# Optimization experiments

Hardware: AMD Instinct MI355X
Metric: run time of the kernel (lower is better)

The kernel has to match this reference:

```python
import jax, jax.numpy as jnp
import numpy as np

L, H, D, V, T, B = 12, 12, 768, 50257, 1024, 2
HD = D // H


def _ln(x, w, b):
    m = jnp.mean(x, axis=-1, keepdims=True)
    v = jnp.var(x, axis=-1, keepdims=True)
    return (x - m) * jax.lax.rsqrt(v + 1e-5) * w + b


def setup_inputs() -> dict:
    key = jax.random.key(0)
    ks = jax.random.split(key, 8)
    def n(k, shape, std=0.02):
        return jax.random.normal(k, shape, jnp.float32) * std
    return dict(
        x=jax.random.randint(ks[0], (B, T), 0, V),
        wte=n(ks[1], (V, D), 0.01),
        wpe=n(ks[2], (T, D), 0.01),
        ln1_w=jnp.ones((L, D), jnp.float32), ln1_b=jnp.zeros((L, D), jnp.float32),
        qkv_w=n(ks[3], (L, D, 3 * D)), qkv_b=jnp.zeros((L, 3 * D), jnp.float32),
        proj_w=n(ks[4], (L, D, D)), proj_b=jnp.zeros((L, D), jnp.float32),
        ln2_w=jnp.ones((L, D), jnp.float32), ln2_b=jnp.zeros((L, D), jnp.float32),
        fc_w=n(ks[5], (L, D, 4 * D)), fc_b=jnp.zeros((L, 4 * D), jnp.float32),
        fcp_w=n(ks[6], (L, 4 * D, D)), fcp_b=jnp.zeros((L, D), jnp.float32),
        lnf_w=jnp.ones((D,), jnp.float32), lnf_b=jnp.zeros((D,), jnp.float32),
    )


def reference(x, wte, wpe, ln1_w, ln1_b, qkv_w, qkv_b, proj_w, proj_b,
              ln2_w, ln2_b, fc_w, fc_b, fcp_w, fcp_b, lnf_w, lnf_b):
    Bn, Tn = x.shape
    h = wte[x] + wpe[:Tn]                                   # [B,T,D]
    mask = jnp.tril(jnp.ones((Tn, Tn), bool))               # causal mask
    scale = 1.0 / np.sqrt(HD).astype(np.float32)

    def block(h, p):
        l1w, l1b, qw, qb, pw, pb, l2w, l2b, fw, fb, p2w, p2b = p
        a = _ln(h, l1w, l1b)
        qkv = a @ qw + qb                                    # [B,T,3D]
        q, k, v = jnp.split(qkv, 3, axis=-1)
        q = q.reshape(Bn, Tn, H, HD)
        k = k.reshape(Bn, Tn, H, HD)
        v = v.reshape(Bn, Tn, H, HD)
        att = jnp.einsum('bqhd,bkhd->bhqk', q, k) * scale    # [B,H,T,T]
        att = jnp.where(mask, att, -jnp.inf)
        att = jax.nn.softmax(att, axis=-1)
        y = jnp.einsum('bhqk,bkhd->bqhd', att, v).reshape(Bn, Tn, D)
        h = h + y @ pw + pb
        m = _ln(h, l2w, l2b)
        m = jax.nn.gelu(m @ fw + fb, approximate=True)       # tanh GELU
        h = h + m @ p2w + p2b
        return h, None

    h, _ = jax.lax.scan(block, h, (ln1_w, ln1_b, qkv_w, qkv_b, proj_w, proj_b,
                                   ln2_w, ln2_b, fc_w, fc_b, fcp_w, fcp_b))
    logits = _ln(h, lnf_w, lnf_b) @ wte.T                    # tied lm_head
    return logits
```

## Files before the change

kernel.cpp:

```cpp
#include <hip/hip_runtime.h>
#include <hip/hip_bf16.h>

typedef __hip_bfloat16 hbf16;
using bf16x8 = __attribute__((ext_vector_type(8))) __bf16;
using f32x4 = __attribute__((ext_vector_type(4))) float;

constexpr int Lc = 12, Hc = 12, Dc = 768, Vc = 50257, Tc = 1024, Bc = 2, HDc = 64;
constexpr int Mc = Bc * Tc;
constexpr int Vpad = 50304;

constexpr size_t SZ_Q = (size_t)3 * Dc * Dc;
constexpr size_t SZ_P = (size_t)Dc * Dc;
constexpr size_t SZ_F = (size_t)4 * Dc * Dc;
constexpr size_t SZ_FP = (size_t)4 * Dc * Dc;
constexpr size_t SZL = SZ_Q + SZ_P + SZ_F + SZ_FP;
constexpr int NPART = Bc * Hc * 8 * 2;

#define GLD16(gp, lp)                                               \
    __builtin_amdgcn_global_load_lds(                               \
        (__attribute__((address_space(1))) void*)(void*)(gp),       \
        (__attribute__((address_space(3))) void*)(void*)(lp), 16, 0, 0)

__global__ void embed_kernel(const int* __restrict__ x, const float* __restrict__ wte,
                             const float* __restrict__ wpe, float* __restrict__ h) {
    int i = blockIdx.x * blockDim.x + threadIdx.x;
    if (i >= Mc * Dc) return;
    int m = i / Dc, d = i - m * Dc;
    int t = m % Tc;
    int tok = x[m];
    h[i] = wte[(size_t)tok * Dc + d] + wpe[(size_t)t * Dc + d];
}

__global__ __launch_bounds__(256) void ln_kernel(const float* __restrict__ x,
                                                 const float* __restrict__ w,
                                                 const float* __restrict__ b,
                                                 hbf16* __restrict__ out) {
    int wv = threadIdx.x >> 6, lane = threadIdx.x & 63;
    int row = blockIdx.x * 4 + wv;
    const float4* xr = (const float4*)(x + (size_t)row * Dc);
    float4 v[3];
    float s = 0.f, sq = 0.f;
#pragma unroll
    for (int i = 0; i < 3; i++) {
        v[i] = xr[i * 64 + lane];
        s += v[i].x + v[i].y + v[i].z + v[i].w;
        sq += v[i].x * v[i].x + v[i].y * v[i].y + v[i].z * v[i].z + v[i].w * v[i].w;
    }
#pragma unroll
    for (int o = 32; o > 0; o >>= 1) {
        s += __shfl_xor(s, o, 64);
        sq += __shfl_xor(sq, o, 64);
    }
    float mean = s * (1.f / Dc);
    float var = sq * (1.f / Dc) - mean * mean;
    float rstd = rsqrtf(var + 1e-5f);
#pragma unroll
    for (int i = 0; i < 3; i++) {
        int c = (i * 64 + lane) * 4;
        float4 wv4 = *(const float4*)(w + c);
        float4 bv4 = *(const float4*)(b + c);
        float r0 = (v[i].x - mean) * rstd * wv4.x + bv4.x;
        float r1 = (v[i].y - mean) * rstd * wv4.y + bv4.y;
        float r2 = (v[i].z - mean) * rstd * wv4.z + bv4.z;
        float r3 = (v[i].w - mean) * rstd * wv4.w + bv4.w;
        __bf16 q0 = (__bf16)r0, q1 = (__bf16)r1, q2 = (__bf16)r2, q3 = (__bf16)r3;
        ushort4 u;
        u.x = *(unsigned short*)&q0; u.y = *(unsigned short*)&q1;
        u.z = *(unsigned short*)&q2; u.w = *(unsigned short*)&q3;
        *(ushort4*)(out + (size_t)row * Dc + c) = u;
    }
}

__global__ __launch_bounds__(256) void transpose4_kernel(
    const float* __restrict__ s0, const float* __restrict__ s1,
    const float* __restrict__ s2, const float* __restrict__ s3,
    hbf16* __restrict__ d0, hbf16* __restrict__ d1,
    hbf16* __restrict__ d2, hbf16* __restrict__ d3) {
    int id = blockIdx.x;
    size_t lz = blockIdx.y;
    int bx, by, K, N;
    const float* W;
    hbf16* Wt;
    if (id < 1728)      { int t = id;        bx = t % 72; by = t / 72; K = 768;  N = 2304; W = s0 + lz * SZ_Q;  Wt = d0 + lz * SZL; }
    else if (id < 2304) { int t = id - 1728; bx = t % 24; by = t / 24; K = 768;  N = 768;  W = s1 + lz * SZ_P;  Wt = d1 + lz * SZL; }
    else if (id < 4608) { int t = id - 2304; bx = t % 96; by = t / 96; K = 768;  N = 3072; W = s2 + lz * SZ_F;  Wt = d2 + lz * SZL; }
    else                { int t = id - 4608; bx = t % 24; by = t / 24; K = 3072; N = 768;  W = s3 + lz * SZ_FP; Wt = d3 + lz * SZL; }

    __shared__ float tile[32][33];
    int n0 = bx * 32, k0 = by * 32;
    int tx = threadIdx.x & 31, ty = threadIdx.x >> 5;
#pragma unroll
    for (int i = 0; i < 4; i++) {
        int r = ty + i * 8;
        tile[r][tx] = W[(size_t)(k0 + r) * N + n0 + tx];
    }
    __syncthreads();
#pragma unroll
    for (int i = 0; i < 4; i++) {
        int r = ty + i * 8;
        Wt[(size_t)(n0 + r) * K + k0 + tx] = __float2bfloat16(tile[tx][r]);
    }
}

__global__ void convert_wte(const float* __restrict__ wte, hbf16* __restrict__ out) {
    size_t i4 = ((size_t)blockIdx.x * 256 + threadIdx.x) * 4;
    if (i4 >= (size_t)Vpad * Dc) return;
    if (i4 < (size_t)Vc * Dc) {
#pragma unroll
        for (int j = 0; j < 4; j++) out[i4 + j] = __float2bfloat16(wte[i4 + j]);
    } else {
#pragma unroll
        for (int j = 0; j < 4; j++) out[i4 + j] = __float2bfloat16(0.f);
    }
}

template <int EPI, bool OUTBF, int BN>
__global__ __launch_bounds__(256) void mm_kernel(const hbf16* __restrict__ A,
                                                 const hbf16* __restrict__ Bt,
                                                 const float* __restrict__ bias,
                                                 const float* __restrict__ resid,
                                                 void* __restrict__ Cout,
                                                 int M, int N, int K) {
    constexpr int NF = BN / 32;
    constexpr int NBI = BN / 32;
    __shared__ __bf16 As[2][64 * 64];
    __shared__ __bf16 Bs[2][BN * 64];
    int tid = threadIdx.x;
    int l = tid & 63, w = tid >> 6;
    int wr = w >> 1, wc = w & 1;

    int gx = gridDim.x, gy = gridDim.y;
    int nwg = gx * gy;
    int hwlin = blockIdx.y * gx + blockIdx.x;
    int wk = (hwlin & 7) * (nwg >> 3) + (hwlin >> 3);
    int m0 = (wk % gy) * 64;
    int n0 = (wk / gy) * BN;

    int sr = tid >> 3, sc = tid & 7;
    int scs = (sc ^ (sr & 7)) * 8;
    const hbf16* pA[2];
#pragma unroll
    for (int j = 0; j < 2; j++) pA[j] = A + (size_t)(m0 + j * 32 + sr) * K + scs;
    const hbf16* pB[NBI];
#pragma unroll
    for (int j = 0; j < NBI; j++) pB[j] = Bt + (size_t)(n0 + j * 32 + sr) * K + scs;

    auto stage = [&](int bi, int ko) {
#pragma unroll
        for (int j = 0; j < 2; j++) GLD16(pA[j] + ko, &As[bi][j * 2048 + tid * 8]);
#pragma unroll
        for (int j = 0; j < NBI; j++) GLD16(pB[j] + ko, &Bs[bi][j * 2048 + tid * 8]);
    };

    int lr = l & 15, lg = l >> 4;
    int aoff[2][2], boff[2][NF];
#pragma unroll
    for (int kk = 0; kk < 2; kk++) {
        int ks = ((kk * 4 + lg) ^ (lr & 7)) * 8;
#pragma unroll
        for (int m = 0; m < 2; m++) aoff[kk][m] = (wr * 32 + m * 16 + lr) * 64 + ks;
#pragma unroll
        for (int n = 0; n < NF; n++) boff[kk][n] = (wc * (BN / 2) + n * 16 + lr) * 64 + ks;
    }

    f32x4 acc[2][NF] = {};
    int nk = K / 64;

    stage(0, 0);
    for (int t = 0; t < nk; ++t) {
        int cur = t & 1;
        if (t + 1 < nk) {
            stage(cur ^ 1, (t + 1) * 64);
            if constexpr (BN == 128)
                asm volatile("s_waitcnt vmcnt(6)" ::: "memory");
            else
                asm volatile("s_waitcnt vmcnt(4)" ::: "memory");
        } else {
            asm volatile("s_waitcnt vmcnt(0)" ::: "memory");
        }
        __builtin_amdgcn_sched_barrier(0);
        __builtin_amdgcn_s_barrier();
        __builtin_amdgcn_sched_barrier(0);
        __builtin_amdgcn_s_setprio(1);
#pragma unroll
        for (int kk = 0; kk < 2; kk++) {
            bf16x8 af[2], bfr[NF];
#pragma unroll
            for (int m = 0; m < 2; m++) af[m] = *(const bf16x8*)&As[cur][aoff[kk][m]];
#pragma unroll
            for (int n = 0; n < NF; n++) bfr[n] = *(const bf16x8*)&Bs[cur][boff[kk][n]];
#pragma unroll
            for (int m = 0; m < 2; m++)
#pragma unroll
                for (int n = 0; n < NF; n++)
                    acc[m][n] = __builtin_amdgcn_mfma_f32_16x16x32_bf16(af[m], bfr[n], acc[m][n], 0, 0, 0);
        }
        __builtin_amdgcn_s_setprio(0);
        __builtin_amdgcn_s_barrier();
    }

#pragma unroll
    for (int n = 0; n < NF; n++) {
        int col = n0 + wc * (BN / 2) + n * 16 + lr;
        bool cok = col < N;
        float bv = (bias && cok) ? bias[col] : 0.f;
#pragma unroll
        for (int m = 0; m < 2; m++) {
#pragma unroll
            for (int r = 0; r < 4; r++) {
                int row = m0 + wr * 32 + m * 16 + lg * 4 + r;
                if (!cok) continue;
                float v = acc[m][n][r] + bv;
                if (EPI == 1) v += resid[(size_t)row * N + col];
                if (EPI == 2) {
                    float x3 = v * v * v;
                    v = 0.5f * v * (1.f + tanhf(0.7978845608028654f * (v + 0.044715f * x3)));
                }
                if (OUTBF)
                    ((hbf16*)Cout)[(size_t)row * N + col] = __float2bfloat16(v);
                else
                    ((float*)Cout)[(size_t)row * N + col] = v;
            }
        }
    }
}

__global__ __launch_bounds__(512) void mm2_kernel(const hbf16* __restrict__ A,
                                                  const hbf16* __restrict__ Bt,
                                                  float* __restrict__ Cout,
                                                  int M, int N, int K) {
    __shared__ __bf16 As[256 * 64];
    __shared__ __bf16 Bs[128 * 64];
    int tid = threadIdx.x;
    int l = tid & 63, w = tid >> 6;
    int wr = w >> 1, wc = w & 1;

    int gx = gridDim.x, gy = gridDim.y;
    int nwg = gx * gy;
    int hwlin = blockIdx.y * gx + blockIdx.x;
    int wk = (hwlin & 7) * (nwg >> 3) + (hwlin >> 3);
    int m0 = (wk & 7) * 256;
    int n0 = (wk >> 3) * 128;

    int sr = tid >> 3, sc = tid & 7;
    int scs = (sc ^ (sr & 7)) * 8;
    const hbf16* pA[4];
    __bf16* lA[4];
#pragma unroll
    for (int j = 0; j < 4; j++) {
        pA[j] = A + (size_t)(m0 + j * 64 + sr) * K + scs;
        lA[j] = As + j * 4096 + tid * 8;
    }
    const hbf16* pB[2];
    __bf16* lB[2];
#pragma unroll
    for (int j = 0; j < 2; j++) {
        pB[j] = Bt + (size_t)(n0 + j * 64 + sr) * K + scs;
        lB[j] = Bs + j * 4096 + tid * 8;
    }

    int lr = l & 15, lg = l >> 4;
    int aoff[2][4], boff[2][4];
#pragma unroll
    for (int kk = 0; kk < 2; kk++) {
        int ks = ((kk * 4 + lg) ^ (lr & 7)) * 8;
#pragma unroll
        for (int m = 0; m < 4; m++) aoff[kk][m] = (wr * 64 + m * 16 + lr) * 64 + ks;
#pragma unroll
        for (int n = 0; n < 4; n++) boff[kk][n] = (wc * 64 + n * 16 + lr) * 64 + ks;
    }

    f32x4 acc[4][4] = {};

    for (int k0 = 0; k0 < K; k0 += 64) {
#pragma unroll
        for (int j = 0; j < 4; j++) {
            GLD16(pA[j], lA[j]);
            pA[j] += 64;
        }
#pragma unroll
        for (int j = 0; j < 2; j++) {
            GLD16(pB[j], lB[j]);
            pB[j] += 64;
        }
        __syncthreads();
        __builtin_amdgcn_s_setprio(1);
#pragma unroll
        for (int kk = 0; kk < 2; kk++) {
            bf16x8 af[4], bfr[4];
#pragma unroll
            for (int m = 0; m < 4; m++) af[m] = *(const bf16x8*)&As[aoff[kk][m]];
#pragma unroll
            for (int n = 0; n < 4; n++) bfr[n] = *(const bf16x8*)&Bs[boff[kk][n]];
#pragma unroll
            for (int m = 0; m < 4; m++)
#pragma unroll
                for (int n = 0; n < 4; n++)
                    acc[m][n] = __builtin_amdgcn_mfma_f32_16x16x32_bf16(af[m], bfr[n], acc[m][n], 0, 0, 0);
        }
        __builtin_amdgcn_s_setprio(0);
        __syncthreads();
    }

#pragma unroll
    for (int n = 0; n < 4; n++) {
        int col = n0 + wc * 64 + n * 16 + lr;
        if (col >= N) continue;
#pragma unroll
        for (int m = 0; m < 4; m++) {
#pragma unroll
            for (int r = 0; r < 4; r++) {
                int row = m0 + wr * 64 + m * 16 + lg * 4 + r;
                Cout[(size_t)row * N + col] = acc[m][n][r];
            }
        }
    }
}

__global__ __launch_bounds__(256) void fattn_kernel(const hbf16* __restrict__ qkv,
                                                    hbf16* __restrict__ y,
                                                    float* __restrict__ part_O,
                                                    float* __restrict__ part_m,
                                                    float* __restrict__ part_l) {
    int s = blockIdx.x;
    int h = blockIdx.y, b = blockIdx.z;
    int qt, jlo, jhi, half = 0;
    bool partial;
    if (s < 16) {
        qt = 8 + (s >> 1);
        half = s & 1;
        int mid = (qt + 1) >> 1;
        jlo = half ? mid : 0;
        jhi = half ? qt : mid - 1;
        partial = true;
    } else {
        qt = s - 16;
        jlo = 0;
        jhi = qt;
        partial = false;
    }
    int q0 = qt * 64;
    int tid = threadIdx.x;
    int l = tid & 63, w = tid >> 6;
    int li = l & 15, lg = l >> 4;
    constexpr int RS = 3 * Dc;
    constexpr int PST = 72;
    constexpr int VST = 72;
    constexpr float SCL = 0.125f * 1.44269504f;
    constexpr float THR = 11.5f;

    __shared__ __bf16 K_lds[2][64 * 64];
    __shared__ __bf16 Vt[2][64 * VST];
    __shared__ __bf16 P_lds[4][16 * PST];

    bf16x8 qf[2];
    {
        const hbf16* qp = qkv + (size_t)(b * Tc + q0 + w * 16 + li) * RS + h * HDc + lg * 8;
        qf[0] = *(const bf16x8*)qp;
        qf[1] = *(const bf16x8*)(qp + 32);
    }

    int krow0 = tid >> 3, krow1 = 32 + (tid >> 3);
    int ks8 = tid & 7;
    int kc0 = (ks8 ^ (krow0 & 7)) * 8;
    int kc1 = (ks8 ^ (krow1 & 7)) * 8;
    const hbf16* kbase = qkv + (size_t)(b * Tc) * RS + Dc + h * HDc;

    int jp = (tid >> 3) * 2;
    int db = (tid & 7) * 8;
    const hbf16* vbase = qkv + (size_t)(b * Tc) * RS + 2 * Dc + h * HDc;

    int koff[2][4];
#pragma unroll
    for (int ks = 0; ks < 2; ks++)
#pragma unroll
        for (int n = 0; n < 4; n++)
            koff[ks][n] = (n * 16 + li) * 64 + (((ks * 4 + lg) ^ (li & 7)) * 8);

    f32x4 acc_o[4] = {};
    float m_run = -1e30f, l_run = 0.f;

    int j0p = jlo * 64;
    bf16x8 vr0, vr1;
    {
        const hbf16* vp = vbase + (size_t)(j0p + jp) * RS + db;
        vr0 = *(const bf16x8*)vp;
        vr1 = *(const bf16x8*)(vp + RS);
        GLD16(kbase + (size_t)(j0p + krow0) * RS + kc0, &K_lds[0][tid * 8]);
        GLD16(kbase + (size_t)(j0p + krow1) * RS + kc1, &K_lds[0][2048 + tid * 8]);
    }
#pragma unroll
    for (int i = 0; i < 8; i++) {
        __bf16 a0 = vr0[i], a1 = vr1[i];
        unsigned u = (unsigned)*(unsigned short*)&a0 | ((unsigned)*(unsigned short*)&a1 << 16);
        *(unsigned*)&Vt[0][(db + i) * VST + jp] = u;
    }

    int cur = 0;
    for (int jt = jlo; jt <= jhi; jt++) {
        int jn0 = (jt < jhi) ? (jt + 1) * 64 : j0p;

        asm volatile("s_waitcnt lgkmcnt(0)" ::: "memory");
        __builtin_amdgcn_s_barrier();

        {
            const hbf16* vp = vbase + (size_t)(jn0 + jp) * RS + db;
            vr0 = *(const bf16x8*)vp;
            vr1 = *(const bf16x8*)(vp + RS);
            GLD16(kbase + (size_t)(jn0 + krow0) * RS + kc0, &K_lds[cur ^ 1][tid * 8]);
            GLD16(kbase + (size_t)(jn0 + krow1) * RS + kc1, &K_lds[cur ^ 1][2048 + tid * 8]);
        }

        asm volatile("s_waitcnt vmcnt(4)" ::: "memory");
        __builtin_amdgcn_sched_barrier(0);

        f32x4 sv[4] = {};
#pragma unroll
        for (int ks = 0; ks < 2; ks++)
#pragma unroll
            for (int n = 0; n < 4; n++) {
                bf16x8 kf = *(const bf16x8*)&K_lds[cur][koff[ks][n]];
                sv[n] = __builtin_amdgcn_mfma_f32_16x16x32_bf16(kf, qf[ks], sv[n], 0, 0, 0);
            }
#pragma unroll
        for (int n = 0; n < 4; n++)
#pragma unroll
            for (int r = 0; r < 4; r++) sv[n][r] *= SCL;

        if (jt == qt) {
            int qloc = w * 16 + li;
#pragma unroll
            for (int n = 0; n < 4; n++)
#pragma unroll
                for (int r = 0; r < 4; r++)
                    if (n * 16 + lg * 4 + r > qloc) sv[n][r] = -1e30f;
        }

        float mx = -1e30f;
#pragma unroll
        for (int n = 0; n < 4; n++)
#pragma unroll
            for (int r = 0; r < 4; r++) mx = fmaxf(mx, sv[n][r]);
        mx = fmaxf(mx, __shfl_xor(mx, 16, 64));
        mx = fmaxf(mx, __shfl_xor(mx, 32, 64));

        bool dfr = __all(mx - m_run <= THR);
        float sclq = 1.f;
        if (!dfr) {
            float mnew = fmaxf(m_run, mx);
            sclq = exp2f(m_run - mnew);
            m_run = mnew;
        }
        float rs = 0.f;
#pragma unroll
        for (int n = 0; n < 4; n++)
#pragma unroll
            for (int r = 0; r < 4; r++) {
                float pv = exp2f(sv[n][r] - m_run);
                sv[n][r] = pv;
                rs += pv;
            }
        rs += __shfl_xor(rs, 16, 64);
        rs += __shfl_xor(rs, 32, 64);
        l_run = (dfr ? l_run : l_run * sclq) + rs;

#pragma unroll
        for (int n = 0; n < 4; n++)
#pragma unroll
            for (int r = 0; r < 4; r += 2) {
                __bf16 b0 = (__bf16)sv[n][r], b1 = (__bf16)sv[n][r + 1];
                unsigned u = (unsigned)*(unsigned short*)&b0 |
                             ((unsigned)*(unsigned short*)&b1 << 16);
                *(unsigned*)&P_lds[w][li * PST + n * 16 + lg * 4 + r] = u;
            }
        bf16x8 pa0 = *(const bf16x8*)&P_lds[w][li * PST + lg * 8];
        bf16x8 pa1 = *(const bf16x8*)&P_lds[w][li * PST + 32 + lg * 8];

        if (!dfr) {
#pragma unroll
            for (int r = 0; r < 4; r++) {
                float sr_ = __shfl(sclq, (l & 48) | (lg * 4 + r), 64);
#pragma unroll
                for (int n2 = 0; n2 < 4; n2++) acc_o[n2][r] *= sr_;
            }
        }

#pragma unroll
        for (int n2 = 0; n2 < 4; n2++) {
            bf16x8 vf0 = *(const bf16x8*)&Vt[cur][(n2 * 16 + li) * VST + lg * 8];
            bf16x8 vf1 = *(const bf16x8*)&Vt[cur][(n2 * 16 + li) * VST + 32 + lg * 8];
            acc_o[n2] = __builtin_amdgcn_mfma_f32_16x16x32_bf16(pa0, vf0, acc_o[n2], 0, 0, 0);
            acc_o[n2] = __builtin_amdgcn_mfma_f32_16x16x32_bf16(pa1, vf1, acc_o[n2], 0, 0, 0);
        }

#pragma unroll
        for (int i = 0; i < 8; i++) {
            __bf16 a0 = vr0[i], a1 = vr1[i];
            unsigned u = (unsigned)*(unsigned short*)&a0 | ((unsigned)*(unsigned short*)&a1 << 16);
            *(unsigned*)&Vt[cur ^ 1][(db + i) * VST + jp] = u;
        }
        cur ^= 1;
    }

    if (partial) {
        int p = ((b * Hc + h) * 8 + (qt - 8)) * 2 + half;
#pragma unroll
        for (int r = 0; r < 4; r++) {
            int lrow = w * 16 + lg * 4 + r;
#pragma unroll
            for (int n2 = 0; n2 < 4; n2++)
                part_O[(size_t)p * 4096 + lrow * 64 + n2 * 16 + li] = acc_o[n2][r];
        }
        if (lg == 0) {
            part_m[p * 64 + w * 16 + li] = m_run;
            part_l[p * 64 + w * 16 + li] = l_run;
        }
    } else {
#pragma unroll
        for (int r = 0; r < 4; r++) {
            float lv = __shfl(l_run, (l & 48) | (lg * 4 + r), 64);
            float rcp = 1.f / lv;
            int row = q0 + w * 16 + lg * 4 + r;
#pragma unroll
            for (int n2 = 0; n2 < 4; n2++)
                y[(size_t)(b * Tc + row) * Dc + h * HDc + n2 * 16 + li] =
                    __float2bfloat16(acc_o[n2][r] * rcp);
        }
    }
}

__global__ __launch_bounds__(256) void fmerge_kernel(const float* __restrict__ part_O,
                                                     const float* __restrict__ part_m,
                                                     const float* __restrict__ part_l,
                                                     hbf16* __restrict__ y) {
    int gi = blockIdx.x * 4 + (threadIdx.x >> 6);
    int lane = threadIdx.x & 63;
    int row512 = gi & 511;
    int bh = gi >> 9;
    int b = bh / Hc, h = bh % Hc;
    int qt8 = row512 >> 6, lrow = row512 & 63;
    int p0 = (bh * 8 + qt8) * 2, p1 = p0 + 1;
    float m0 = part_m[p0 * 64 + lrow], m1 = part_m[p1 * 64 + lrow];
    float l0 = part_l[p0 * 64 + lrow], l1 = part_l[p1 * 64 + lrow];
    float m = fmaxf(m0, m1);
    float a0 = exp2f(m0 - m), a1 = exp2f(m1 - m);
    float lsum = l0 * a0 + l1 * a1;
    float o0 = part_O[(size_t)p0 * 4096 + lrow * 64 + lane];
    float o1 = part_O[(size_t)p1 * 4096 + lrow * 64 + lane];
    float o = (o0 * a0 + o1 * a1) / lsum;
    int q = (8 + qt8) * 64 + lrow;
    y[((size_t)b * Tc + q) * Dc + h * HDc + lane] = __float2bfloat16(o);
}

extern "C" void kernel_launch(void* const* d_in, const int* in_sizes, int n_in,
                              void* d_out, int out_size, void* d_ws, size_t ws_size,
                              hipStream_t stream) {
    const int* x = (const int*)d_in[0];
    const float* wte = (const float*)d_in[1];
    const float* wpe = (const float*)d_in[2];
    const float* ln1w = (const float*)d_in[3];
    const float* ln1b = (const float*)d_in[4];
    const float* qkvw = (const float*)d_in[5];
    const float* qkvb = (const float*)d_in[6];
    const float* projw = (const float*)d_in[7];
    const float* projb = (const float*)d_in[8];
    const float* ln2w = (const float*)d_in[9];
    const float* ln2b = (const float*)d_in[10];
    const float* fcw = (const float*)d_in[11];
    const float* fcb = (const float*)d_in[12];
    const float* fcpw = (const float*)d_in[13];
    const float* fcpb = (const float*)d_in[14];
    const float* lnfw = (const float*)d_in[15];
    const float* lnfb = (const float*)d_in[16];

    char* p = (char*)d_ws;
    float* h = (float*)p;      p += (size_t)Mc * Dc * 4;
    hbf16* qkv = (hbf16*)p;    p += (size_t)Mc * 3 * Dc * 2;
    hbf16* a = (hbf16*)p;      p += (size_t)Mc * Dc * 2;
    hbf16* y = (hbf16*)p;      p += (size_t)Mc * Dc * 2;
    hbf16* mlp = (hbf16*)p;    p += (size_t)Mc * 4 * Dc * 2;
    hbf16* wte_b = (hbf16*)p;  p += (size_t)Vpad * Dc * 2;
    float* part_O = (float*)p; p += (size_t)NPART * 4096 * 4;
    float* part_m = (float*)p; p += (size_t)NPART * 64 * 4;
    float* part_l = (float*)p; p += (size_t)NPART * 64 * 4;
    hbf16* wtr = (hbf16*)p;
    size_t used = (size_t)((char*)wtr - (char*)d_ws);
    bool all_mode = (ws_size - used) >= (size_t)Lc * SZL * 2;

    embed_kernel<<<(Mc * Dc + 255) / 256, 256, 0, stream>>>(x, wte, wpe, h);
    convert_wte<<<((size_t)Vpad * Dc / 4 + 255) / 256, 256, 0, stream>>>(wte, wte_b);

    if (all_mode) {
        transpose4_kernel<<<dim3(6912, Lc), 256, 0, stream>>>(
            qkvw, projw, fcw, fcpw,
            wtr, wtr + SZ_Q, wtr + SZ_Q + SZ_P, wtr + SZ_Q + SZ_P + SZ_F);
    }

    for (int l = 0; l < Lc; l++) {
        hbf16* base = wtr + (all_mode ? (size_t)l * SZL : 0);
        hbf16* wq_t = base;
        hbf16* wp_t = base + SZ_Q;
        hbf16* wf_t = base + SZ_Q + SZ_P;
        hbf16* wfp_t = base + SZ_Q + SZ_P + SZ_F;
        if (!all_mode) {
            transpose4_kernel<<<dim3(6912, 1), 256, 0, stream>>>(
                qkvw + (size_t)l * SZ_Q, projw + (size_t)l * SZ_P,
                fcw + (size_t)l * SZ_F, fcpw + (size_t)l * SZ_FP,
                wq_t, wp_t, wf_t, wfp_t);
        }

        ln_kernel<<<Mc / 4, 256, 0, stream>>>(h, ln1w + (size_t)l * Dc, ln1b + (size_t)l * Dc, a);
        mm_kernel<0, true, 128><<<dim3(3 * Dc / 128, Mc / 64), 256, 0, stream>>>(
            a, wq_t, qkvb + (size_t)l * 3 * Dc, nullptr, qkv, Mc, 3 * Dc, Dc);
        fattn_kernel<<<dim3(24, Hc, Bc), 256, 0, stream>>>(qkv, y, part_O, part_m, part_l);
        fmerge_kernel<<<Bc * Hc * 512 / 4, 256, 0, stream>>>(part_O, part_m, part_l, y);
        mm_kernel<1, false, 64><<<dim3(Dc / 64, Mc / 64), 256, 0, stream>>>(
            y, wp_t, projb + (size_t)l * Dc, h, h, Mc, Dc, Dc);
        ln_kernel<<<Mc / 4, 256, 0, stream>>>(h, ln2w + (size_t)l * Dc, ln2b + (size_t)l * Dc, a);
        mm_kernel<2, true, 128><<<dim3(4 * Dc / 128, Mc / 64), 256, 0, stream>>>(
            a, wf_t, fcb + (size_t)l * 4 * Dc, nullptr, mlp, Mc, 4 * Dc, Dc);
        mm_kernel<1, false, 64><<<dim3(Dc / 64, Mc / 64), 256, 0, stream>>>(
            mlp, wfp_t, fcpb + (size_t)l * Dc, h, h, Mc, Dc, 4 * Dc);
    }

    ln_kernel<<<Mc / 4, 256, 0, stream>>>(h, lnfw, lnfb, a);
    mm2_kernel<<<dim3(Vpad / 128, Mc / 256), 512, 0, stream>>>(
        a, wte_b, (float*)d_out, Mc, Vc, Dc);
}
```

Before: 2.060 ms.

## Fuse split-KV attention merge into attention kernel via atomic ticket

Drops the separate fmerge kernel launch. Each pair of split-KV partial blocks in the attention kernel now takes an atomic ticket, and whichever block finishes second reads both partials and writes the merged output. A per-layer counter array is cleared once with a memset at the start. This saves one launch and its dependency bubble per layer, at the cost of a threadfence and atomic in the attention tail. Separately, the s_setprio raise/lower around the GEMM MFMA loop is removed.

Result: slower. 2.843 ms (+38.0%).

```diff
diff --git a/kernel.cpp b/kernel.cpp
--- a/kernel.cpp
+++ b/kernel.cpp
@@ -15,6 +15,7 @@
 constexpr size_t SZ_FP = (size_t)4 * Dc * Dc;
 constexpr size_t SZL = SZ_Q + SZ_P + SZ_F + SZ_FP;
 constexpr int NPART = Bc * Hc * 8 * 2;
+constexpr int NCNT = Bc * Hc * 8;
 
 #define GLD16(gp, lp)                                               \
     __builtin_amdgcn_global_load_lds(                               \
@@ -181,7 +182,6 @@
         __builtin_amdgcn_sched_barrier(0);
         __builtin_amdgcn_s_barrier();
         __builtin_amdgcn_sched_barrier(0);
-        __builtin_amdgcn_s_setprio(1);
 #pragma unroll
         for (int kk = 0; kk < 2; kk++) {
             bf16x8 af[2], bfr[NF];
@@ -195,7 +195,6 @@
                 for (int n = 0; n < NF; n++)
                     acc[m][n] = __builtin_amdgcn_mfma_f32_16x16x32_bf16(af[m], bfr[n], acc[m][n], 0, 0, 0);
         }
-        __builtin_amdgcn_s_setprio(0);
         __builtin_amdgcn_s_barrier();
     }
 
@@ -321,7 +320,8 @@
                                                     hbf16* __restrict__ y,
                                                     float* __restrict__ part_O,
                                                     float* __restrict__ part_m,
-                                                    float* __restrict__ part_l) {
+                                                    float* __restrict__ part_l,
+                                                    int* __restrict__ cnt) {
     int s = blockIdx.x;
     int h = blockIdx.y, b = blockIdx.z;
     int qt, jlo, jhi, half = 0;
@@ -352,6 +352,7 @@
     __shared__ __bf16 K_lds[2][64 * 64];
     __shared__ __bf16 Vt[2][64 * VST];
     __shared__ __bf16 P_lds[4][16 * PST];
+    __shared__ int ticket;
 
     bf16x8 qf[2];
     {
@@ -503,17 +504,40 @@
     }
 
     if (partial) {
-        int p = ((b * Hc + h) * 8 + (qt - 8)) * 2 + half;
+        int bh = b * Hc + h;
+        int pi = bh * 8 + (qt - 8);
+        int p0 = pi * 2, pme = p0 + half;
 #pragma unroll
         for (int r = 0; r < 4; r++) {
             int lrow = w * 16 + lg * 4 + r;
 #pragma unroll
             for (int n2 = 0; n2 < 4; n2++)
-                part_O[(size_t)p * 4096 + lrow * 64 + n2 * 16 + li] = acc_o[n2][r];
+                part_O[(size_t)pme * 4096 + lrow * 64 + n2 * 16 + li] = acc_o[n2][r];
         }
         if (lg == 0) {
-            part_m[p * 64 + w * 16 + li] = m_run;
-            part_l[p * 64 + w * 16 + li] = l_run;
+            part_m[pme * 64 + w * 16 + li] = m_run;
+            part_l[pme * 64 + w * 16 + li] = l_run;
+        }
+        __syncthreads();
+        __threadfence();
+        if (tid == 0) ticket = atomicAdd(&cnt[pi], 1);
+        __syncthreads();
+        if (ticket == 1) {
+            __threadfence();
+            int p1 = p0 + 1;
+#pragma unroll 4
+            for (int rr = 0; rr < 16; rr++) {
+                int lrow = w * 16 + rr;
+                float m0v = part_m[p0 * 64 + lrow], m1v = part_m[p1 * 64 + lrow];
+                float l0v = part_l[p0 * 64 + lrow], l1v = part_l[p1 * 64 + lrow];
+                float mm_ = fmaxf(m0v, m1v);
+                float a0 = exp2f(m0v - mm_), a1 = exp2f(m1v - mm_);
+                float lsum = l0v * a0 + l1v * a1;
+                float o0 = part_O[(size_t)p0 * 4096 + lrow * 64 + l];
+                float o1 = part_O[(size_t)p1 * 4096 + lrow * 64 + l];
+                float o = (o0 * a0 + o1 * a1) / lsum;
+                y[((size_t)b * Tc + q0 + lrow) * Dc + h * HDc + l] = __float2bfloat16(o);
+            }
         }
     } else {
 #pragma unroll
@@ -527,29 +551,6 @@
                     __float2bfloat16(acc_o[n2][r] * rcp);
         }
     }
-}
-
-__global__ __launch_bounds__(256) void fmerge_kernel(const float* __restrict__ part_O,
-                                                     const float* __restrict__ part_m,
-                                                     const float* __restrict__ part_l,
-                                                     hbf16* __restrict__ y) {
-    int gi = blockIdx.x * 4 + (threadIdx.x >> 6);
-    int lane = threadIdx.x & 63;
-    int row512 = gi & 511;
-    int bh = gi >> 9;
-    int b = bh / Hc, h = bh % Hc;
-    int qt8 = row512 >> 6, lrow = row512 & 63;
-    int p0 = (bh * 8 + qt8) * 2, p1 = p0 + 1;
-    float m0 = part_m[p0 * 64 + lrow], m1 = part_m[p1 * 64 + lrow];
-    float l0 = part_l[p0 * 64 + lrow], l1 = part_l[p1 * 64 + lrow];
-    float m = fmaxf(m0, m1);
-    float a0 = exp2f(m0 - m), a1 = exp2f(m1 - m);
-    float lsum = l0 * a0 + l1 * a1;
-    float o0 = part_O[(size_t)p0 * 4096 + lrow * 64 + lane];
-    float o1 = part_O[(size_t)p1 * 4096 + lrow * 64 + lane];
-    float o = (o0 * a0 + o1 * a1) / lsum;
-    int q = (8 + qt8) * 64 + lrow;
-    y[((size_t)b * Tc + q) * Dc + h * HDc + lane] = __float2bfloat16(o);
 }
 
 extern "C" void kernel_launch(void* const* d_in, const int* in_sizes, int n_in,
@@ -583,10 +584,12 @@
     float* part_O = (float*)p; p += (size_t)NPART * 4096 * 4;
     float* part_m = (float*)p; p += (size_t)NPART * 64 * 4;
     float* part_l = (float*)p; p += (size_t)NPART * 64 * 4;
+    int* cnt = (int*)p;        p += (size_t)Lc * NCNT * 4;
     hbf16* wtr = (hbf16*)p;
     size_t used = (size_t)((char*)wtr - (char*)d_ws);
     bool all_mode = (ws_size - used) >= (size_t)Lc * SZL * 2;
 
+    hipMemsetAsync(cnt, 0, (size_t)Lc * NCNT * 4, stream);
     embed_kernel<<<(Mc * Dc + 255) / 256, 256, 0, stream>>>(x, wte, wpe, h);
     convert_wte<<<((size_t)Vpad * Dc / 4 + 255) / 256, 256, 0, stream>>>(wte, wte_b);
 
@@ -612,8 +615,8 @@
         ln_kernel<<<Mc / 4, 256, 0, stream>>>(h, ln1w + (size_t)l * Dc, ln1b + (size_t)l * Dc, a);
         mm_kernel<0, true, 128><<<dim3(3 * Dc / 128, Mc / 64), 256, 0, stream>>>(
             a, wq_t, qkvb + (size_t)l * 3 * Dc, nullptr, qkv, Mc, 3 * Dc, Dc);
-        fattn_kernel<<<dim3(24, Hc, Bc), 256, 0, stream>>>(qkv, y, part_O, part_m, part_l);
-        fmerge_kernel<<<Bc * Hc * 512 / 4, 256, 0, stream>>>(part_O, part_m, part_l, y);
+        fattn_kernel<<<dim3(24, Hc, Bc), 256, 0, stream>>>(
+            qkv, y, part_O, part_m, part_l, cnt + l * NCNT);
         mm_kernel<1, false, 64><<<dim3(Dc / 64, Mc / 64), 256, 0, stream>>>(
             y, wp_t, projb + (size_t)l * Dc, h, h, Mc, Dc, Dc);
         ln_kernel<<<Mc / 4, 256, 0, stream>>>(h, ln2w + (size_t)l * Dc, ln2b + (size_t)l * Dc, a);
```
